# Optimization experiments

Measured on AMD Instinct MI355X. Metric: run time of the kernel, lower is better.

The kernel has to match this reference:

```python
import jax, jax.numpy as jnp
import numpy as np

N_EMBD = 1024
N_HEAD = 16
LORA_R = 8
LORA_ALPHA = 16
SCALE = LORA_ALPHA / LORA_R


def lora_linear(x, W, b, A, Bm):
    # loralib: F.linear(x, W, b) + (x @ A.T @ B.T) * scaling
    return x @ W.T + b + ((x @ A.T) @ Bm.T) * SCALE


def setup_inputs() -> dict:
    key = jax.random.key(0)
    ks = jax.random.split(key, 9)
    B, T, C = 4, 2048, N_EMBD
    s_in = 1.0 / np.sqrt(C)
    x = jax.random.normal(ks[0], (B, T, C), dtype=jnp.float32)
    Wqkv = jax.random.normal(ks[1], (3 * C, C), dtype=jnp.float32) * s_in
    bqkv = jnp.zeros((3 * C,), dtype=jnp.float32)
    Aqkv = jax.random.normal(ks[2], (LORA_R, C), dtype=jnp.float32) * s_in
    Bqkv = jnp.zeros((3 * C, LORA_R), dtype=jnp.float32)  # loralib inits B to zero
    Wproj = jax.random.normal(ks[3], (C, C), dtype=jnp.float32) * s_in
    bproj = jnp.zeros((C,), dtype=jnp.float32)
    Aproj = jax.random.normal(ks[4], (LORA_R, C), dtype=jnp.float32) * s_in
    Bproj = jnp.zeros((C, LORA_R), dtype=jnp.float32)
    return {"x": x, "Wqkv": Wqkv, "bqkv": bqkv, "Aqkv": Aqkv, "Bqkv": Bqkv,
            "Wproj": Wproj, "bproj": bproj, "Aproj": Aproj, "Bproj": Bproj}


def reference(x, Wqkv, bqkv, Aqkv, Bqkv, Wproj, bproj, Aproj, Bproj):
    B, T, C = x.shape
    H, D = N_HEAD, C // N_HEAD
    qkv = lora_linear(x, Wqkv, bqkv, Aqkv, Bqkv)  # [B,T,3C]
    q, k, v = jnp.split(qkv, 3, axis=2)
    # [B,T,C] -> [B,H,T,D]
    q = q.reshape(B, T, H, D).transpose(0, 2, 1, 3)
    k = k.reshape(B, T, H, D).transpose(0, 2, 1, 3)
    v = v.reshape(B, T, H, D).transpose(0, 2, 1, 3)
    att = jnp.einsum("bhqd,bhkd->bhqk", q, k) * (1.0 / np.sqrt(D))
    causal = jnp.tril(jnp.ones((T, T), dtype=bool))
    att = jnp.where(causal[None, None], att, jnp.float32(-jnp.inf))
    att = jax.nn.softmax(att, axis=-1)
    out = jnp.einsum("bhqk,bhkd->bhqd", att, v)  # [B,H,T,D]
    out = out.transpose(0, 2, 1, 3).reshape(B, T, C)
    return lora_linear(out, Wproj, bproj, Aproj, Bproj)
```

## Files before the change

### kernel.cpp

```cpp
#include <hip/hip_runtime.h>
#include <hip/hip_bf16.h>

typedef __bf16 bf16_t;
typedef __bf16 bf16x8 __attribute__((ext_vector_type(8)));
typedef float  f32x4  __attribute__((ext_vector_type(4)));

#define MFMA_BF16 __builtin_amdgcn_mfma_f32_16x16x32_bf16
#define NEG_BIG  (-3.0e38f)

__device__ __forceinline__ void load16_lds(const bf16_t* g, bf16_t* l) {
    __builtin_amdgcn_global_load_lds(
        (const __attribute__((address_space(1))) void*)g,
        (__attribute__((address_space(3))) void*)l, 16, 0, 0);
}

__device__ inline bf16x8 ld8(const bf16_t* p) { return *(const bf16x8*)p; }
__device__ inline bf16x8 ld8(const float* p) {
    f32x4 a = *(const f32x4*)p;
    f32x4 b = *(const f32x4*)(p + 4);
    bf16x8 o;
    o[0] = (bf16_t)a[0]; o[1] = (bf16_t)a[1]; o[2] = (bf16_t)a[2]; o[3] = (bf16_t)a[3];
    o[4] = (bf16_t)b[0]; o[5] = (bf16_t)b[1]; o[6] = (bf16_t)b[2]; o[7] = (bf16_t)b[3];
    return o;
}

__global__ __launch_bounds__(256) void cvt_f32_bf16(
    const float* __restrict__ in, bf16_t* __restrict__ out)
{
    size_t i = ((size_t)blockIdx.x * 256 + threadIdx.x) * 8;
    *(bf16x8*)&out[i] = ld8(&in[i]);
}

template <typename TX>
__global__ __launch_bounds__(256) void lora_xa_kernel(
    const TX* __restrict__ X, const float* __restrict__ A,
    float* __restrict__ out)
{
    const int lane = threadIdx.x & 63;
    const int w    = threadIdx.x >> 6;
    const int m    = blockIdx.x * 4 + w;
    const TX* xp = X + (size_t)m * 1024;

    float acc[8];
#pragma unroll
    for (int r = 0; r < 8; r++) acc[r] = 0.f;

#pragma unroll 4
    for (int ci = 0; ci < 16; ci++) {
        int k = ci * 64 + lane;
        float xv = (float)xp[k];
#pragma unroll
        for (int r = 0; r < 8; r++) acc[r] += xv * A[r * 1024 + k];
    }
#pragma unroll
    for (int r = 0; r < 8; r++) {
        float v = acc[r];
        v += __shfl_xor(v, 1);  v += __shfl_xor(v, 2);  v += __shfl_xor(v, 4);
        v += __shfl_xor(v, 8);  v += __shfl_xor(v, 16); v += __shfl_xor(v, 32);
        if (lane == 0) out[m * 8 + r] = v;
    }
}

__device__ __forceinline__ void gemm_epilogue(
    f32x4 (&acc)[4][4], const float* bias, const float* xA, const float* LB,
    bf16_t* C0, bf16_t* C1, bf16_t* C2, float* Cf,
    int tile_m, int tile_n, int wm, int wn, int c, int g)
{
    const int seg    = tile_n >> 10;
    const int tn_loc = tile_n & 1023;
    bf16_t* Cout = (seg == 0) ? C0 : (seg == 1) ? C1 : C2;

    float biasf[4];
    float lbv[4][8];
#pragma unroll
    for (int j = 0; j < 4; j++) {
        int col = tile_n + wn + j * 16 + c;
        biasf[j] = bias[col];
        f32x4 lb0 = *(const f32x4*)&LB[(size_t)col * 8];
        f32x4 lb1 = *(const f32x4*)&LB[(size_t)col * 8 + 4];
#pragma unroll
        for (int r = 0; r < 4; r++) { lbv[j][r] = lb0[r]; lbv[j][r + 4] = lb1[r]; }
    }
#pragma unroll
    for (int i = 0; i < 4; i++) {
#pragma unroll
        for (int rg = 0; rg < 4; rg++) {
            int row = tile_m + wm + i * 16 + g * 4 + rg;
            f32x4 xa0 = *(const f32x4*)&xA[(size_t)row * 8];
            f32x4 xa1 = *(const f32x4*)&xA[(size_t)row * 8 + 4];
#pragma unroll
            for (int j = 0; j < 4; j++) {
                float lora = xa0[0] * lbv[j][0] + xa0[1] * lbv[j][1] +
                             xa0[2] * lbv[j][2] + xa0[3] * lbv[j][3] +
                             xa1[0] * lbv[j][4] + xa1[1] * lbv[j][5] +
                             xa1[2] * lbv[j][6] + xa1[3] * lbv[j][7];
                float v = acc[i][j][rg] + biasf[j] + 2.0f * lora;
                int lcol = tn_loc + wn + j * 16 + c;
                if (Cf) Cf[(size_t)row * 1024 + lcol] = v;
                else    Cout[(size_t)row * 1024 + lcol] = (bf16_t)v;
            }
        }
    }
}

template <typename TA, typename TW>
__global__ __launch_bounds__(256) void gemm_bias_lora(
    const TA* __restrict__ A, const TW* __restrict__ W,
    const float* __restrict__ bias, const float* __restrict__ xA,
    const float* __restrict__ LB,
    bf16_t* __restrict__ C0, bf16_t* __restrict__ C1, bf16_t* __restrict__ C2,
    float* __restrict__ Cf, int K)
{
    __shared__ __align__(16) bf16_t As[128 * 72];
    __shared__ __align__(16) bf16_t Bs[128 * 72];

    const int t    = threadIdx.x;
    const int lane = t & 63;
    const int w    = t >> 6;
    const int wm   = (w >> 1) * 64;
    const int wn   = (w & 1) * 64;
    const int c    = lane & 15;
    const int g    = lane >> 4;
    const int tile_m = blockIdx.y * 128;
    const int tile_n = blockIdx.x * 128;

    const int srow = t >> 3;
    const int scol = (t & 7) * 8;

    f32x4 acc[4][4];
#pragma unroll
    for (int i = 0; i < 4; i++)
#pragma unroll
        for (int j = 0; j < 4; j++) {
            f32x4 z = {0.f, 0.f, 0.f, 0.f};
            acc[i][j] = z;
        }

    for (int k0 = 0; k0 < K; k0 += 64) {
#pragma unroll
        for (int i = 0; i < 4; i++) {
            int r = srow + i * 32;
            *(bf16x8*)&As[r * 72 + scol] = ld8(&A[(size_t)(tile_m + r) * K + k0 + scol]);
            *(bf16x8*)&Bs[r * 72 + scol] = ld8(&W[(size_t)(tile_n + r) * K + k0 + scol]);
        }
        __syncthreads();

#pragma unroll
        for (int kk = 0; kk < 2; kk++) {
            bf16x8 af[4], bfr[4];
#pragma unroll
            for (int i = 0; i < 4; i++)
                af[i] = *(const bf16x8*)&As[(wm + i * 16 + c) * 72 + kk * 32 + g * 8];
#pragma unroll
            for (int j = 0; j < 4; j++)
                bfr[j] = *(const bf16x8*)&Bs[(wn + j * 16 + c) * 72 + kk * 32 + g * 8];
#pragma unroll
            for (int i = 0; i < 4; i++)
#pragma unroll
                for (int j = 0; j < 4; j++)
                    acc[i][j] = MFMA_BF16(af[i], bfr[j], acc[i][j], 0, 0, 0);
        }
        __syncthreads();
    }
    gemm_epilogue(acc, bias, xA, LB, C0, C1, C2, Cf, tile_m, tile_n, wm, wn, c, g);
}

#define AS_OFF(row, q) ((row) * 64 + (((q) ^ ((row) & 7)) * 8))

__global__ __launch_bounds__(256) void gemm_async(
    const bf16_t* __restrict__ A, const bf16_t* __restrict__ W,
    const float* __restrict__ bias, const float* __restrict__ xA,
    const float* __restrict__ LB,
    bf16_t* __restrict__ C0, bf16_t* __restrict__ C1, bf16_t* __restrict__ C2,
    float* __restrict__ Cf, int K)
{
    __shared__ __align__(16) bf16_t As[128 * 64];
    __shared__ __align__(16) bf16_t Bs[128 * 64];

    const int t    = threadIdx.x;
    const int lane = t & 63;
    const int w    = t >> 6;
    const int wm   = (w >> 1) * 64;
    const int wn   = (w & 1) * 64;
    const int c    = lane & 15;
    const int g    = lane >> 4;
    const int tile_m = blockIdx.y * 128;
    const int tile_n = blockIdx.x * 128;

    const int trow = t >> 3;
    const int k8   = (t & 7) ^ (trow & 7);
    const bf16_t* Ab = A + (size_t)tile_m * K + k8 * 8;
    const bf16_t* Wb = W + (size_t)tile_n * K + k8 * 8;

    f32x4 acc[4][4];
#pragma unroll
    for (int i = 0; i < 4; i++)
#pragma unroll
        for (int j = 0; j < 4; j++) {
            f32x4 z = {0.f, 0.f, 0.f, 0.f};
            acc[i][j] = z;
        }

    for (int k0 = 0; k0 < K; k0 += 64) {
#pragma unroll
        for (int i = 0; i < 4; i++) {
            int row = i * 32 + trow;
            load16_lds(&Ab[(size_t)row * K + k0], &As[(i * 256 + t) * 8]);
            load16_lds(&Wb[(size_t)row * K + k0], &Bs[(i * 256 + t) * 8]);
        }
        __syncthreads();

#pragma unroll
        for (int kk = 0; kk < 2; kk++) {
            bf16x8 af[4], bfr[4];
#pragma unroll
            for (int i = 0; i < 4; i++)
                af[i] = *(const bf16x8*)&As[AS_OFF(wm + i * 16 + c, kk * 4 + g)];
#pragma unroll
            for (int j = 0; j < 4; j++)
                bfr[j] = *(const bf16x8*)&Bs[AS_OFF(wn + j * 16 + c, kk * 4 + g)];
#pragma unroll
            for (int i = 0; i < 4; i++)
#pragma unroll
                for (int j = 0; j < 4; j++)
                    acc[i][j] = MFMA_BF16(af[i], bfr[j], acc[i][j], 0, 0, 0);
        }
        __syncthreads();
    }
    gemm_epilogue(acc, bias, xA, LB, C0, C1, C2, Cf, tile_m, tile_n, wm, wn, c, g);
}

#define VT_IDX(d, kv) ((d) * 72 + ((d) >> 4) * 8 + (kv))
#define PS_IDX(q, kv) ((q) * 72 + ((q) >> 2) * 8 + (kv))
#define PW_REGION 1168

__global__ __launch_bounds__(256) void attn_kernel(
    bf16_t* __restrict__ Q, const bf16_t* __restrict__ Kg,
    const bf16_t* __restrict__ Vg)
{
    __shared__ __align__(16) bf16_t Ks[64 * 72];
    __shared__ __align__(16) bf16_t Vt[64 * 72 + 32];
    __shared__ __align__(16) bf16_t Ps[4 * PW_REGION];

    const int t    = threadIdx.x;
    const int lane = t & 63;
    const int w    = t >> 6;
    const int c    = lane & 15;
    const int g    = lane >> 4;

    const int id = blockIdx.x;
    const int qb = 31 - (id >> 6);
    const int h  = id & 15;
    const int b  = (id >> 4) & 3;
    const int q0 = qb * 64;
    const size_t base = (size_t)b * 2048 * 1024;

    bf16x8 qf[2];
    {
        int qrow = q0 + w * 16 + c;
        const bf16_t* qp = Q + base + (size_t)qrow * 1024 + h * 64;
        qf[0] = *(const bf16x8*)&qp[g * 8];
        qf[1] = *(const bf16x8*)&qp[32 + g * 8];
    }

    bf16x8 ones;
#pragma unroll
    for (int e = 0; e < 8; e++) ones[e] = (bf16_t)1.0f;

    f32x4 acc_o[4];
#pragma unroll
    for (int jd = 0; jd < 4; jd++) {
        f32x4 z = {0.f, 0.f, 0.f, 0.f};
        acc_o[jd] = z;
    }
    f32x4 acc_l = {0.f, 0.f, 0.f, 0.f};
    float m_run[4];
#pragma unroll
    for (int r = 0; r < 4; r++) m_run[r] = NEG_BIG;

    const int sr = t >> 2;
    const int sc = (t & 3) * 16;
    const int vtbase = VT_IDX(sc, sr);

    bf16x8 kr0, kr1, vr0, vr1;
    {
        const bf16_t* kp = Kg + base + (size_t)sr * 1024 + h * 64 + sc;
        kr0 = *(const bf16x8*)&kp[0];
        kr1 = *(const bf16x8*)&kp[8];
        const bf16_t* vp = Vg + base + (size_t)sr * 1024 + h * 64 + sc;
        vr0 = *(const bf16x8*)&vp[0];
        vr1 = *(const bf16x8*)&vp[8];
    }

    for (int kt = 0; kt <= qb; kt++) {
        if (kt > 0) __syncthreads();
        *(bf16x8*)&Ks[sr * 72 + sc]     = kr0;
        *(bf16x8*)&Ks[sr * 72 + sc + 8] = kr1;
#pragma unroll
        for (int e = 0; e < 8; e++) Vt[vtbase + e * 72]       = vr0[e];
#pragma unroll
        for (int e = 0; e < 8; e++) Vt[vtbase + (e + 8) * 72] = vr1[e];
        __syncthreads();

        if (kt < qb) {
            const bf16_t* kp = Kg + base + (size_t)((kt + 1) * 64 + sr) * 1024 + h * 64 + sc;
            kr0 = *(const bf16x8*)&kp[0];
            kr1 = *(const bf16x8*)&kp[8];
            const bf16_t* vp = Vg + base + (size_t)((kt + 1) * 64 + sr) * 1024 + h * 64 + sc;
            vr0 = *(const bf16x8*)&vp[0];
            vr1 = *(const bf16x8*)&vp[8];
        }

        f32x4 s[4];
#pragma unroll
        for (int j = 0; j < 4; j++) {
            f32x4 z = {0.f, 0.f, 0.f, 0.f};
            s[j] = z;
        }
#pragma unroll
        for (int kk = 0; kk < 2; kk++) {
            bf16x8 kf[4];
#pragma unroll
            for (int j = 0; j < 4; j++)
                kf[j] = *(const bf16x8*)&Ks[(j * 16 + c) * 72 + kk * 32 + g * 8];
#pragma unroll
            for (int j = 0; j < 4; j++)
                s[j] = MFMA_BF16(qf[kk], kf[j], s[j], 0, 0, 0);
        }

        float sv[4][4];
#pragma unroll
        for (int j = 0; j < 4; j++)
#pragma unroll
            for (int r = 0; r < 4; r++) sv[j][r] = s[j][r] * 0.125f;

        if (kt == qb) {
#pragma unroll
            for (int j = 0; j < 4; j++) {
                int kv = j * 16 + c;
#pragma unroll
                for (int r = 0; r < 4; r++) {
                    int q = w * 16 + g * 4 + r;
                    if (kv > q) sv[j][r] = NEG_BIG;
                }
            }
        }

        float alpha[4];
#pragma unroll
        for (int r = 0; r < 4; r++) {
            float mx = fmaxf(fmaxf(sv[0][r], sv[1][r]), fmaxf(sv[2][r], sv[3][r]));
            mx = fmaxf(mx, __shfl_xor(mx, 1));
            mx = fmaxf(mx, __shfl_xor(mx, 2));
            mx = fmaxf(mx, __shfl_xor(mx, 4));
            mx = fmaxf(mx, __shfl_xor(mx, 8));
            float mnew = fmaxf(m_run[r], mx);
            alpha[r] = __expf(m_run[r] - mnew);
            m_run[r] = mnew;
        }
        float pv[4][4];
#pragma unroll
        for (int j = 0; j < 4; j++)
#pragma unroll
            for (int r = 0; r < 4; r++) pv[j][r] = __expf(sv[j][r] - m_run[r]);

        bf16_t* Pw = &Ps[w * PW_REGION];
#pragma unroll
        for (int j = 0; j < 4; j++)
#pragma unroll
            for (int r = 0; r < 4; r++)
                Pw[(g * 4 + r) * 72 + g * 8 + j * 16 + c] = (bf16_t)pv[j][r];

#pragma unroll
        for (int jd = 0; jd < 4; jd++)
#pragma unroll
            for (int r = 0; r < 4; r++) acc_o[jd][r] *= alpha[r];
#pragma unroll
        for (int r = 0; r < 4; r++) acc_l[r] *= alpha[r];

#pragma unroll
        for (int kkv = 0; kkv < 2; kkv++) {
            bf16x8 pf = *(const bf16x8*)&Pw[PS_IDX(c, kkv * 32 + g * 8)];
#pragma unroll
            for (int jd = 0; jd < 4; jd++) {
                bf16x8 vf = *(const bf16x8*)&Vt[VT_IDX(jd * 16 + c, kkv * 32 + g * 8)];
                acc_o[jd] = MFMA_BF16(pf, vf, acc_o[jd], 0, 0, 0);
            }
            acc_l = MFMA_BF16(pf, ones, acc_l, 0, 0, 0);
        }
    }

#pragma unroll
    for (int jd = 0; jd < 4; jd++) {
#pragma unroll
        for (int r = 0; r < 4; r++) {
            int qrow = q0 + w * 16 + g * 4 + r;
            float v = acc_o[jd][r] / acc_l[r];
            Q[base + (size_t)qrow * 1024 + h * 64 + jd * 16 + c] = (bf16_t)v;
        }
    }
}

extern "C" void kernel_launch(void* const* d_in, const int* in_sizes, int n_in,
                              void* d_out, int out_size, void* d_ws, size_t ws_size,
                              hipStream_t stream) {
    const float* x     = (const float*)d_in[0];
    const float* Wqkv  = (const float*)d_in[1];
    const float* bqkv  = (const float*)d_in[2];
    const float* Aqkv  = (const float*)d_in[3];
    const float* Bqkv  = (const float*)d_in[4];
    const float* Wproj = (const float*)d_in[5];
    const float* bproj = (const float*)d_in[6];
    const float* Aproj = (const float*)d_in[7];
    const float* Bproj = (const float*)d_in[8];
    float* out = (float*)d_out;

    char* ws = (char*)d_ws;
    const size_t MB = 1024 * 1024;
    const bool big = ws_size >= (size_t)(72.5 * 1024 * 1024) + 65536;

    if (big) {
        float*  xa1    = (float*)ws;
        float*  xa2    = (float*)(ws + 262144);
        bf16_t* x16    = (bf16_t*)(ws + 524288);
        bf16_t* Wqkv16 = x16 + (size_t)8192 * 1024;
        bf16_t* Wproj16= Wqkv16 + (size_t)3072 * 1024;
        bf16_t* Qfull  = Wproj16 + (size_t)1024 * 1024;
        bf16_t* Kfull  = Qfull + (size_t)8192 * 1024;
        bf16_t* Vfull  = Kfull + (size_t)8192 * 1024;

        cvt_f32_bf16<<<4096, 256, 0, stream>>>(x, x16);
        cvt_f32_bf16<<<1536, 256, 0, stream>>>(Wqkv, Wqkv16);
        cvt_f32_bf16<<< 512, 256, 0, stream>>>(Wproj, Wproj16);

        lora_xa_kernel<bf16_t><<<2048, 256, 0, stream>>>(x16, Aqkv, xa1);

        gemm_async<<<dim3(24, 64), 256, 0, stream>>>(
            x16, Wqkv16, bqkv, xa1, Bqkv, Qfull, Kfull, Vfull, nullptr, 1024);

        attn_kernel<<<2048, 256, 0, stream>>>(Qfull, Kfull, Vfull);

        lora_xa_kernel<bf16_t><<<2048, 256, 0, stream>>>(Qfull, Aproj, xa2);

        gemm_async<<<dim3(8, 64), 256, 0, stream>>>(
            Qfull, Wproj16, bproj, xa2, Bproj,
            nullptr, nullptr, nullptr, out, 1024);
    } else {
        float*  xa1   = (float*)ws;
        float*  xa2   = (float*)(ws + 262144);
        bf16_t* Qfull = (bf16_t*)(ws + 524288);
        bf16_t* Kfull = Qfull + (size_t)8192 * 1024;
        bf16_t* Vfull = Kfull + (size_t)8192 * 1024;

        lora_xa_kernel<float><<<2048, 256, 0, stream>>>(x, Aqkv, xa1);
        gemm_bias_lora<float, float><<<dim3(24, 64), 256, 0, stream>>>(
            x, Wqkv, bqkv, xa1, Bqkv, Qfull, Kfull, Vfull, nullptr, 1024);
        attn_kernel<<<2048, 256, 0, stream>>>(Qfull, Kfull, Vfull);
        lora_xa_kernel<bf16_t><<<2048, 256, 0, stream>>>(Qfull, Aproj, xa2);
        gemm_bias_lora<bf16_t, float><<<dim3(8, 64), 256, 0, stream>>>(
            Qfull, Wproj, bproj, xa2, Bproj,
            nullptr, nullptr, nullptr, out, 1024);
    }
    (void)MB;
}
```

Measured before the change: 339.3 us.

## Fuse prep conversions with LoRA-xA and restructure attention softmax with lazy rescale

```diff
diff --git a/kernel.cpp b/kernel.cpp
--- a/kernel.cpp
+++ b/kernel.cpp
@@ -3,10 +3,17 @@
 
 typedef __bf16 bf16_t;
 typedef __bf16 bf16x8 __attribute__((ext_vector_type(8)));
+typedef __bf16 bf16x4 __attribute__((ext_vector_type(4)));
 typedef float  f32x4  __attribute__((ext_vector_type(4)));
 
 #define MFMA_BF16 __builtin_amdgcn_mfma_f32_16x16x32_bf16
 #define NEG_BIG  (-3.0e38f)
+
+#if __has_builtin(__builtin_amdgcn_exp2f)
+#define EXP2F(x) __builtin_amdgcn_exp2f(x)
+#else
+#define EXP2F(x) exp2f(x)
+#endif
 
 __device__ __forceinline__ void load16_lds(const bf16_t* g, bf16_t* l) {
     __builtin_amdgcn_global_load_lds(
@@ -24,23 +31,12 @@
     return o;
 }
 
-__global__ __launch_bounds__(256) void cvt_f32_bf16(
-    const float* __restrict__ in, bf16_t* __restrict__ out)
-{
-    size_t i = ((size_t)blockIdx.x * 256 + threadIdx.x) * 8;
-    *(bf16x8*)&out[i] = ld8(&in[i]);
-}
-
 template <typename TX>
-__global__ __launch_bounds__(256) void lora_xa_kernel(
+__device__ __forceinline__ void lora_xa_body(
     const TX* __restrict__ X, const float* __restrict__ A,
-    float* __restrict__ out)
-{
-    const int lane = threadIdx.x & 63;
-    const int w    = threadIdx.x >> 6;
-    const int m    = blockIdx.x * 4 + w;
+    float* __restrict__ out, int m, int lane)
+{
     const TX* xp = X + (size_t)m * 1024;
-
     float acc[8];
 #pragma unroll
     for (int r = 0; r < 8; r++) acc[r] = 0.f;
@@ -58,6 +54,40 @@
         v += __shfl_xor(v, 1);  v += __shfl_xor(v, 2);  v += __shfl_xor(v, 4);
         v += __shfl_xor(v, 8);  v += __shfl_xor(v, 16); v += __shfl_xor(v, 32);
         if (lane == 0) out[m * 8 + r] = v;
+    }
+}
+
+template <typename TX>
+__global__ __launch_bounds__(256) void lora_xa_kernel(
+    const TX* __restrict__ X, const float* __restrict__ A,
+    float* __restrict__ out)
+{
+    const int lane = threadIdx.x & 63;
+    const int w    = threadIdx.x >> 6;
+    const int m    = blockIdx.x * 4 + w;
+    lora_xa_body<TX>(X, A, out, m, lane);
+}
+
+__global__ __launch_bounds__(256) void prep_kernel(
+    const float* __restrict__ x, const float* __restrict__ Wqkv,
+    const float* __restrict__ Wproj,
+    bf16_t* __restrict__ x16, bf16_t* __restrict__ Wqkv16,
+    bf16_t* __restrict__ Wproj16,
+    const float* __restrict__ Aqkv, float* __restrict__ xa1)
+{
+    const int bid = blockIdx.x;
+    if (bid < 6144) {
+        const float* in; bf16_t* out; size_t off;
+        if (bid < 4096)      { in = x;     out = x16;     off = (size_t)bid * 2048; }
+        else if (bid < 5632) { in = Wqkv;  out = Wqkv16;  off = (size_t)(bid - 4096) * 2048; }
+        else                 { in = Wproj; out = Wproj16; off = (size_t)(bid - 5632) * 2048; }
+        size_t i = off + (size_t)threadIdx.x * 8;
+        *(bf16x8*)&out[i] = ld8(&in[i]);
+    } else {
+        const int lane = threadIdx.x & 63;
+        const int w    = threadIdx.x >> 6;
+        const int m    = (bid - 6144) * 4 + w;
+        lora_xa_body<float>(x, Aqkv, xa1, m, lane);
     }
 }
 
@@ -234,7 +264,7 @@
 #define PS_IDX(q, kv) ((q) * 72 + ((q) >> 2) * 8 + (kv))
 #define PW_REGION 1168
 
-__global__ __launch_bounds__(256) void attn_kernel(
+__global__ __launch_bounds__(256, 4) void attn_kernel(
     bf16_t* __restrict__ Q, const bf16_t* __restrict__ Kg,
     const bf16_t* __restrict__ Vg)
 {
@@ -274,9 +304,7 @@
         acc_o[jd] = z;
     }
     f32x4 acc_l = {0.f, 0.f, 0.f, 0.f};
-    float m_run[4];
-#pragma unroll
-    for (int r = 0; r < 4; r++) m_run[r] = NEG_BIG;
+    float m_run = NEG_BIG;
 
     const int sr = t >> 2;
     const int sc = (t & 3) * 16;
@@ -325,58 +353,58 @@
                 kf[j] = *(const bf16x8*)&Ks[(j * 16 + c) * 72 + kk * 32 + g * 8];
 #pragma unroll
             for (int j = 0; j < 4; j++)
-                s[j] = MFMA_BF16(qf[kk], kf[j], s[j], 0, 0, 0);
-        }
-
-        float sv[4][4];
+                s[j] = MFMA_BF16(kf[j], qf[kk], s[j], 0, 0, 0);
+        }
+
+        const float SCL = 0.125f * 1.44269504088896f;
 #pragma unroll
         for (int j = 0; j < 4; j++)
 #pragma unroll
-            for (int r = 0; r < 4; r++) sv[j][r] = s[j][r] * 0.125f;
+            for (int r = 0; r < 4; r++) s[j][r] *= SCL;
 
         if (kt == qb) {
 #pragma unroll
-            for (int j = 0; j < 4; j++) {
-                int kv = j * 16 + c;
-#pragma unroll
-                for (int r = 0; r < 4; r++) {
-                    int q = w * 16 + g * 4 + r;
-                    if (kv > q) sv[j][r] = NEG_BIG;
-                }
-            }
-        }
-
-        float alpha[4];
-#pragma unroll
-        for (int r = 0; r < 4; r++) {
-            float mx = fmaxf(fmaxf(sv[0][r], sv[1][r]), fmaxf(sv[2][r], sv[3][r]));
-            mx = fmaxf(mx, __shfl_xor(mx, 1));
-            mx = fmaxf(mx, __shfl_xor(mx, 2));
-            mx = fmaxf(mx, __shfl_xor(mx, 4));
-            mx = fmaxf(mx, __shfl_xor(mx, 8));
-            float mnew = fmaxf(m_run[r], mx);
-            alpha[r] = __expf(m_run[r] - mnew);
-            m_run[r] = mnew;
-        }
-        float pv[4][4];
+            for (int j = 0; j < 4; j++)
+#pragma unroll
+                for (int r = 0; r < 4; r++)
+                    if (j * 16 + g * 4 + r > w * 16 + c) s[j][r] = NEG_BIG;
+        }
+
+        float mx;
+        {
+            float a0 = fmaxf(fmaxf(s[0][0], s[0][1]), fmaxf(s[0][2], s[0][3]));
+            float a1 = fmaxf(fmaxf(s[1][0], s[1][1]), fmaxf(s[1][2], s[1][3]));
+            float a2 = fmaxf(fmaxf(s[2][0], s[2][1]), fmaxf(s[2][2], s[2][3]));
+            float a3 = fmaxf(fmaxf(s[3][0], s[3][1]), fmaxf(s[3][2], s[3][3]));
+            mx = fmaxf(fmaxf(a0, a1), fmaxf(a2, a3));
+            mx = fmaxf(mx, __shfl_xor(mx, 16));
+            mx = fmaxf(mx, __shfl_xor(mx, 32));
+        }
+
+        if (!__all(mx <= m_run + 8.0f)) {
+            float mnew  = fmaxf(m_run, mx);
+            float alpha = EXP2F(m_run - mnew);
+            m_run = mnew;
+#pragma unroll
+            for (int jd = 0; jd < 4; jd++)
+#pragma unroll
+                for (int r = 0; r < 4; r++) acc_o[jd][r] *= alpha;
+            acc_l[0] *= alpha;
+        }
+
 #pragma unroll
         for (int j = 0; j < 4; j++)
 #pragma unroll
-            for (int r = 0; r < 4; r++) pv[j][r] = __expf(sv[j][r] - m_run[r]);
+            for (int r = 0; r < 4; r++) s[j][r] = EXP2F(s[j][r] - m_run);
 
         bf16_t* Pw = &Ps[w * PW_REGION];
 #pragma unroll
-        for (int j = 0; j < 4; j++)
-#pragma unroll
-            for (int r = 0; r < 4; r++)
-                Pw[(g * 4 + r) * 72 + g * 8 + j * 16 + c] = (bf16_t)pv[j][r];
-
-#pragma unroll
-        for (int jd = 0; jd < 4; jd++)
-#pragma unroll
-            for (int r = 0; r < 4; r++) acc_o[jd][r] *= alpha[r];
-#pragma unroll
-        for (int r = 0; r < 4; r++) acc_l[r] *= alpha[r];
+        for (int j = 0; j < 4; j++) {
+            bf16x4 pk;
+#pragma unroll
+            for (int r = 0; r < 4; r++) pk[r] = (bf16_t)s[j][r];
+            *(bf16x4*)&Pw[PS_IDX(c, j * 16 + g * 4)] = pk;
+        }
 
 #pragma unroll
         for (int kkv = 0; kkv < 2; kkv++) {
@@ -384,20 +412,21 @@
 #pragma unroll
             for (int jd = 0; jd < 4; jd++) {
                 bf16x8 vf = *(const bf16x8*)&Vt[VT_IDX(jd * 16 + c, kkv * 32 + g * 8)];
-                acc_o[jd] = MFMA_BF16(pf, vf, acc_o[jd], 0, 0, 0);
+                acc_o[jd] = MFMA_BF16(vf, pf, acc_o[jd], 0, 0, 0);
             }
-            acc_l = MFMA_BF16(pf, ones, acc_l, 0, 0, 0);
-        }
-    }
-
+            acc_l = MFMA_BF16(ones, pf, acc_l, 0, 0, 0);
+        }
+    }
+
+    float rl = 1.0f / acc_l[0];
+    int qrow = q0 + w * 16 + c;
+    bf16_t* op = Q + base + (size_t)qrow * 1024 + h * 64;
 #pragma unroll
     for (int jd = 0; jd < 4; jd++) {
-#pragma unroll
-        for (int r = 0; r < 4; r++) {
-            int qrow = q0 + w * 16 + g * 4 + r;
-            float v = acc_o[jd][r] / acc_l[r];
-            Q[base + (size_t)qrow * 1024 + h * 64 + jd * 16 + c] = (bf16_t)v;
-        }
+        bf16x4 o4;
+#pragma unroll
+        for (int r = 0; r < 4; r++) o4[r] = (bf16_t)(acc_o[jd][r] * rl);
+        *(bf16x4*)&op[jd * 16 + g * 4] = o4;
     }
 }
 
@@ -416,7 +445,6 @@
     float* out = (float*)d_out;
 
     char* ws = (char*)d_ws;
-    const size_t MB = 1024 * 1024;
     const bool big = ws_size >= (size_t)(72.5 * 1024 * 1024) + 65536;
 
     if (big) {
@@ -429,11 +457,8 @@
         bf16_t* Kfull  = Qfull + (size_t)8192 * 1024;
         bf16_t* Vfull  = Kfull + (size_t)8192 * 1024;
 
-        cvt_f32_bf16<<<4096, 256, 0, stream>>>(x, x16);
-        cvt_f32_bf16<<<1536, 256, 0, stream>>>(Wqkv, Wqkv16);
-        cvt_f32_bf16<<< 512, 256, 0, stream>>>(Wproj, Wproj16);
-
-        lora_xa_kernel<bf16_t><<<2048, 256, 0, stream>>>(x16, Aqkv, xa1);
+        prep_kernel<<<8192, 256, 0, stream>>>(
+            x, Wqkv, Wproj, x16, Wqkv16, Wproj16, Aqkv, xa1);
 
         gemm_async<<<dim3(24, 64), 256, 0, stream>>>(
             x16, Wqkv16, bqkv, xa1, Bqkv, Qfull, Kfull, Vfull, nullptr, 1024);
@@ -461,5 +486,4 @@
             Qfull, Wproj, bproj, xa2, Bproj,
             nullptr, nullptr, nullptr, out, 1024);
     }
-    (void)MB;
-}
+}
```

After: 315.8 us. 6.9% less time.
